# Kernel tuning notes

Measured on AMD Instinct MI355X. Metric: run time of the kernel, lower is better.

The kernel has to match this reference:

```python
import jax, jax.numpy as jnp
import numpy as np

D_MODEL = 256
D_IN = (D_MODEL + 1) ** 2  # 66049


def setup_inputs() -> dict:
    key = jax.random.key(0)
    k1, k2, k3, k4 = jax.random.split(key, 4)
    X = jax.random.normal(k1, (16, 256, 256), dtype=jnp.float32)
    X_aux = jax.random.normal(k2, (16, 256, 256), dtype=jnp.float32)
    # nn.Linear params: weight [out, in], bias [out]
    W = jax.random.normal(k3, (D_MODEL, D_IN), dtype=jnp.float32) / np.sqrt(D_IN)
    b = jax.random.normal(k4, (D_MODEL,), dtype=jnp.float32) * 0.01
    return {"X": X, "X_aux": X_aux, "W": W, "b": b}


def reference(X, X_aux, W, b):
    bsz, t, d = X.shape
    ones = jnp.ones((bsz, t, 1), dtype=X.dtype)
    Xa = jnp.concatenate([ones, X], axis=2)        # [b, t, d+1]
    Xb = jnp.concatenate([ones, X_aux], axis=2)    # [b, t, d+1]
    # outer product per (b, t): [b, t, d+1, d+1]
    tf = jnp.einsum("bti,btj->btij", Xa, Xb)
    tf = tf.reshape(bsz, t, -1)                    # [b, t, (d+1)^2]
    out = jnp.einsum("btk,ok->bto", tf, W) + b     # [b, t, d_model]
    return out
```

## Files before the change

### kernel.cpp

```cpp
#include <hip/hip_runtime.h>
#include <hip/hip_bf16.h>


#define DI 66049

typedef __attribute__((ext_vector_type(8))) short bf16x8;
typedef __attribute__((ext_vector_type(4))) float f32x4;

__device__ __forceinline__ unsigned short f2b(float f) {
  union { __hip_bfloat16 h; unsigned short u; } cv;
  cv.h = __float2bfloat16(f);
  return cv.u;
}

__device__ __forceinline__ bf16x8 pack8(f32x4 lo, f32x4 hi) {
  bf16x8 r;
  r[0] = (short)f2b(lo[0]); r[1] = (short)f2b(lo[1]);
  r[2] = (short)f2b(lo[2]); r[3] = (short)f2b(lo[3]);
  r[4] = (short)f2b(hi[0]); r[5] = (short)f2b(hi[1]);
  r[6] = (short)f2b(hi[2]); r[7] = (short)f2b(hi[3]);
  return r;
}

__device__ __forceinline__ void gload16(const void* g, void* l) {
  __builtin_amdgcn_global_load_lds(
      (const __attribute__((address_space(1))) unsigned int*)g,
      (__attribute__((address_space(3))) unsigned int*)l, 16, 0, 0);
}

__global__ void prep_w(const float* __restrict__ W, unsigned short* __restrict__ Bp) {
  const int c = blockIdx.x;
  const int o = (blockIdx.y << 2) + (threadIdx.x >> 6);
  const int j = (threadIdx.x & 63) << 2;
  const float* wrow = W + (size_t)o * DI;
  float v0, v1, v2, v3;
  if (c < 256) {
    const int bse = (c + 1) * 257 + 1 + j;
    v0 = wrow[bse]; v1 = wrow[bse + 1]; v2 = wrow[bse + 2]; v3 = wrow[bse + 3];
  } else if (c == 256) {
    const int bse = 1 + j;
    v0 = wrow[bse]; v1 = wrow[bse + 1]; v2 = wrow[bse + 2]; v3 = wrow[bse + 3];
  } else {
    v0 = wrow[(j + 1) * 257]; v1 = wrow[(j + 2) * 257];
    v2 = wrow[(j + 3) * 257]; v3 = wrow[(j + 4) * 257];
  }
  unsigned short* dst = Bp + (((size_t)c << 8) + o) * 256 + j;
  const unsigned int lo = (unsigned int)f2b(v0) | ((unsigned int)f2b(v1) << 16);
  const unsigned int hi = (unsigned int)f2b(v2) | ((unsigned int)f2b(v3) << 16);
  *(uint2*)dst = make_uint2(lo, hi);
}

__global__ void prep_xt(const float* __restrict__ X, float* __restrict__ Xt) {
  __shared__ float t[32][33];
  const int tx = threadIdx.x, ty = threadIdx.y;
  const int bt0 = blockIdx.x << 5, c0 = blockIdx.y << 5;
#pragma unroll
  for (int k = 0; k < 4; ++k) {
    const int row = (ty << 2) + k;
    t[row][tx] = X[(size_t)(bt0 + row) * 256 + c0 + tx];
  }
  __syncthreads();
#pragma unroll
  for (int k = 0; k < 4; ++k) {
    const int row = (ty << 2) + k;
    Xt[(size_t)(c0 + row) * 4096 + bt0 + tx] = t[tx][row];
  }
}

#define PACK_AS(SRC)                                                           \
  {                                                                            \
    const int _row = tid >> 2, _q = tid & 3;                                   \
    const float* _rp = (SRC) + (size_t)(bt0 + _row) * 256 + (_q << 6);         \
    const int _sx = _row & 15;                                                 \
    _Pragma("unroll") for (int _w = 0; _w < 8; ++_w) {                         \
      f32x4 _lo = *(const f32x4*)(_rp + (_w << 3));                            \
      f32x4 _hi = *(const f32x4*)(_rp + (_w << 3) + 4);                        \
      const int _slot = (_q << 3) + _w;                                        \
      *(bf16x8*)(&As[_row * 256 + ((_slot ^ _sx) << 3)]) = pack8(_lo, _hi);    \
    }                                                                          \
  }

#define LOAD_AFC()                                                             \
  {                                                                            \
    _Pragma("unroll") for (int _k4 = 0; _k4 < 2; ++_k4) {                      \
      _Pragma("unroll") for (int _rg = 0; _rg < 4; ++_rg) {                    \
        const int _ra = wr + (_rg << 4) + l15;                                 \
        const int _sx = _ra & 15;                                              \
        const int _sb = _k4 << 3;                                              \
        afc[_k4][_rg][0] =                                                     \
            *(const bf16x8*)(&As[_ra * 256 + (((_sb + lg) ^ _sx) << 3)]);      \
        afc[_k4][_rg][1] =                                                     \
            *(const bf16x8*)(&As[_ra * 256 + (((_sb + 4 + lg) ^ _sx) << 3)]);  \
      }                                                                        \
    }                                                                          \
  }

#define STAGE(C, JB, BUF)                                                      \
  {                                                                            \
    const unsigned _cb = ((unsigned)(C) << 16) + (unsigned)(JB);               \
    _Pragma("unroll") for (int _e = 0; _e < 4; ++_e) {                         \
      gload16(Bp + _cb + stg_off[_e],                                          \
              &Bs[BUF][(size_t)(((_e << 9) | tid)) << 3]);                     \
    }                                                                          \
  }

#define NEXT_CJ(K4, CN, JBN)                                                   \
  int _nk = (ci << 2) + (K4) + 1;                                              \
  if (_nk > nkmax) _nk = nkmax;                                                \
  const int _nci = _nk >> 2;                                                   \
  const int CN = is7 ? (_nci < 32 ? 225 + _nci : 257) : c0 + _nci;             \
  const int JBN = (_nk & 3) << 6;

#define KT(K4, CUR, A0X, A1X)                                                  \
  {                                                                            \
    NEXT_CJ(K4, _cn, _jbn);                                                    \
    STAGE(_cn, _jbn, (CUR) ^ 1);                                               \
    bf16x8 bf0[4], bf1[4];                                                     \
    _Pragma("unroll") for (int fn = 0; fn < 4; ++fn) {                         \
      const int _rb = (wn << 6) + (fn << 4) + l15;                             \
      const int _rx = _rb & 7;                                                 \
      bf0[fn] = *(const bf16x8*)(&Bs[CUR][_rb * 64 + ((lg ^ _rx) << 3)]);      \
      bf1[fn] = *(const bf16x8*)(&Bs[CUR][_rb * 64 + (((4 + lg) ^ _rx) << 3)]);\
    }                                                                          \
    _Pragma("unroll") for (int rg = 0; rg < 4; ++rg) {                         \
      bf16x8 _a0 = (A0X);                                                      \
      bf16x8 _a1 = (A1X);                                                      \
      _Pragma("unroll") for (int fn = 0; fn < 4; ++fn) {                       \
        t[rg][fn] = __builtin_amdgcn_mfma_f32_16x16x32_bf16(_a0, bf0[fn],      \
                                                            t[rg][fn], 0, 0, 0); \
        t[rg][fn] = __builtin_amdgcn_mfma_f32_16x16x32_bf16(_a1, bf1[fn],      \
                                                            t[rg][fn], 0, 0, 0); \
      }                                                                        \
    }                                                                          \
    __syncthreads();                                                           \
  }

#define ALDS(K4, HALF)                                                         \
  (*(const bf16x8*)(&As[(wr + (rg << 4) + l15) * 256 +                         \
                        (((((K4) << 3) + (HALF)*4 + lg) ^                      \
                          ((wr + (rg << 4) + l15) & 15))                       \
                         << 3)]))

__global__ __launch_bounds__(512, 1) void gemm_r8(
    const float* __restrict__ X, const float* __restrict__ Xb,
    const float* __restrict__ Xt, const unsigned short* __restrict__ Bp,
    float* __restrict__ P) {
  __shared__ __align__(16) unsigned short As[128 * 256];
  __shared__ __align__(16) unsigned short Bs[2][256 * 64];

  const int tid = threadIdx.x;
  const int rid = blockIdx.x;
  const int slice = rid & 7;
  const int bx = rid >> 3;
  const int bt0 = bx << 7;
  const bool is7 = (slice == 7);
  const int c0 = is7 ? 225 : slice * 32 + (slice ? 1 : 0);
  const int nCh = (slice == 0 || is7) ? 33 : 32;
  const int nkmax = (nCh << 2) - 1;

  const int wid = tid >> 6, lane = tid & 63;
  const int wm = wid >> 2, wn = wid & 3;
  const int wr = wm << 6;
  const int l15 = lane & 15, lg = lane >> 4;

  unsigned stg_off[4];
#pragma unroll
  for (int e = 0; e < 4; ++e) {
    const int row = (e << 6) | (tid >> 3);
    const int sl = (tid & 7) ^ (row & 7);
    stg_off[e] = (unsigned)(row * 256 + (sl << 3));
  }

  PACK_AS(Xb);
  STAGE(c0, 0, 0);
  __syncthreads();

  bf16x8 afc[2][4][2];
  LOAD_AFC();

  f32x4 acc[4][4] = {};

  for (int ci = 0; ci < nCh; ++ci) {
    const int c = is7 ? (ci < 32 ? 225 + ci : 257) : c0 + ci;

    f32x4 t[4][4] = {};
    KT(0, 0, afc[0][rg][0], afc[0][rg][1]);
    KT(1, 1, afc[1][rg][0], afc[1][rg][1]);
    KT(2, 0, ALDS(2, 0), ALDS(2, 1));
    KT(3, 1, ALDS(3, 0), ALDS(3, 1));

    f32x4 s4[4];
    if (c < 256) {
      const float* sp = Xt + (size_t)c * 4096 + bt0 + wr + (lg << 2);
#pragma unroll
      for (int rg = 0; rg < 4; ++rg) s4[rg] = *(const f32x4*)(sp + (rg << 4));
    } else {
#pragma unroll
      for (int rg = 0; rg < 4; ++rg) s4[rg] = (f32x4){1.f, 1.f, 1.f, 1.f};
    }
#pragma unroll
    for (int rg = 0; rg < 4; ++rg)
#pragma unroll
      for (int fn = 0; fn < 4; ++fn) acc[rg][fn] += s4[rg] * t[rg][fn];

    if (is7 && ci == 31) {
      __syncthreads();
      PACK_AS(X);
      __syncthreads();
      LOAD_AFC();
    }
  }

  float* pp = P + ((size_t)slice << 20);
#pragma unroll
  for (int rg = 0; rg < 4; ++rg) {
    const int row = bt0 + wr + (rg << 4) + (lg << 2);
#pragma unroll
    for (int fn = 0; fn < 4; ++fn) {
      const int col = (wn << 6) + (fn << 4) + l15;
#pragma unroll
      for (int e = 0; e < 4; ++e)
        pp[(size_t)(row + e) * 256 + col] = acc[rg][fn][e];
    }
  }
}

__global__ void reduce_k(const float* __restrict__ P, const float* __restrict__ W,
                         const float* __restrict__ b, float* __restrict__ out,
                         int nsl) {
  const int idx = blockIdx.x * 256 + threadIdx.x;
  const int o = idx & 255;
  float v = b[o] + W[(size_t)o * DI];
  for (int s = 0; s < nsl; ++s) v += P[idx + (size_t)s * 1048576];
  out[idx] = v;
}

__global__ void init_k(const float* __restrict__ W, const float* __restrict__ b,
                       float* __restrict__ out) {
  const int idx = blockIdx.x * 256 + threadIdx.x;
  const int o = idx & 255;
  out[idx] = b[o] + W[(size_t)o * DI];
}

__global__ __launch_bounds__(256, 4) void gemm_fb(
    const float* __restrict__ X, const float* __restrict__ Xa,
    const float* __restrict__ W, float* __restrict__ Out) {
  __shared__ __align__(16) unsigned short Asf[128 * 64];
  __shared__ __align__(16) unsigned short Bsf[128 * 64];
  const int tid = threadIdx.x;
  const int bx = blockIdx.x, by = blockIdx.y, bz = blockIdx.z;
  const int S = gridDim.z;
  const int bt0 = bx << 7, o0 = by << 7;
  const int q = 258 / S, r = 258 % S;
  const int c0 = bz * q + (bz < r ? bz : r);
  const int ccnt = q + (bz < r ? 1 : 0);
  const int nK = ccnt << 2;
  const int wid = tid >> 6, lane = tid & 63;
  const int wr = (wid >> 1) << 6, wc = (wid & 1) << 6;
  const int ar = tid >> 1;
  const int ah = (tid & 1) << 5;
  const float* xrow = X + (size_t)(bt0 + ar) * 256;
  const float* varow = Xa + (size_t)(bt0 + ar) * 256;
  f32x4 acc[4][4] = {};
  for (int kt = 0; kt < nK; ++kt) {
    const int c = c0 + (kt >> 2);
    const int j0 = (kt & 3) << 6;
    __syncthreads();
    {
      const float* vs = (c == 257) ? xrow : varow;
      float s = 1.0f;
      if (c < 256) s = xrow[c];
      const f32x4* vp = (const f32x4*)(vs + j0 + ah);
      f32x4 v[8];
#pragma unroll
      for (int qq = 0; qq < 8; ++qq) v[qq] = vp[qq];
      unsigned short* aw = Asf + ar * 64;
      const int sl0 = ah >> 3, sx = ar & 7;
#pragma unroll
      for (int w = 0; w < 4; ++w) {
        bf16x8 pk;
#pragma unroll
        for (int e = 0; e < 8; ++e)
          pk[e] = (short)f2b(s * v[w * 2 + (e >> 2)][e & 3]);
        *(bf16x8*)(aw + (((sl0 + w) ^ sx) << 3)) = pk;
      }
    }
    {
      const int orow = tid >> 1;
      const int jh = (tid & 1) << 5;
      const float* wrow = W + (size_t)(o0 + orow) * DI;
      float tmp[32];
      if (c < 256) {
        const int bse = (c + 1) * 257 + 1 + j0 + jh;
#pragma unroll
        for (int i = 0; i < 32; ++i) tmp[i] = wrow[bse + i];
      } else if (c == 256) {
        const int bse = 1 + j0 + jh;
#pragma unroll
        for (int i = 0; i < 32; ++i) tmp[i] = wrow[bse + i];
      } else {
#pragma unroll
        for (int i = 0; i < 32; ++i) tmp[i] = wrow[(j0 + jh + i + 1) * 257];
      }
      unsigned short* bw = Bsf + orow * 64;
      const int sl0 = jh >> 3, sx = orow & 7;
#pragma unroll
      for (int w = 0; w < 4; ++w) {
        bf16x8 pk;
#pragma unroll
        for (int e = 0; e < 8; ++e) pk[e] = (short)f2b(tmp[w * 8 + e]);
        *(bf16x8*)(bw + (((sl0 + w) ^ sx) << 3)) = pk;
      }
    }
    __syncthreads();
#pragma unroll
    for (int kk = 0; kk < 2; ++kk) {
      const int kslot = (kk << 2) + (lane >> 4);
      bf16x8 af[4], bfr2[4];
#pragma unroll
      for (int fm = 0; fm < 4; ++fm) {
        const int row = wr + (fm << 4) + (lane & 15);
        af[fm] = *(const bf16x8*)(Asf + row * 64 + ((kslot ^ (row & 7)) << 3));
      }
#pragma unroll
      for (int fn = 0; fn < 4; ++fn) {
        const int row = wc + (fn << 4) + (lane & 15);
        bfr2[fn] = *(const bf16x8*)(Bsf + row * 64 + ((kslot ^ (row & 7)) << 3));
      }
#pragma unroll
      for (int fm = 0; fm < 4; ++fm)
#pragma unroll
        for (int fn = 0; fn < 4; ++fn)
          acc[fm][fn] = __builtin_amdgcn_mfma_f32_16x16x32_bf16(
              af[fm], bfr2[fn], acc[fm][fn], 0, 0, 0);
    }
  }
  const int r0 = (lane >> 4) << 2;
  const int cl = lane & 15;
#pragma unroll
  for (int fm = 0; fm < 4; ++fm) {
    const int row = bt0 + wr + (fm << 4) + r0;
#pragma unroll
    for (int fn = 0; fn < 4; ++fn) {
      const int col = o0 + wc + (fn << 4) + cl;
#pragma unroll
      for (int rr = 0; rr < 4; ++rr)
        atomicAdd(Out + (size_t)(row + rr) * 256 + col, acc[fm][fn][rr]);
    }
  }
}

extern "C" void kernel_launch(void* const* d_in, const int* in_sizes, int n_in,
                              void* d_out, int out_size, void* d_ws, size_t ws_size,
                              hipStream_t stream) {
  const float* X  = (const float*)d_in[0];
  const float* Xa = (const float*)d_in[1];
  const float* W  = (const float*)d_in[2];
  const float* b  = (const float*)d_in[3];
  float* out = (float*)d_out;

  const size_t WBF_SZ = (size_t)258 * 256 * 256 * 2;
  const size_t XT_SZ  = (size_t)256 * 4096 * 4;
  const size_t PART1  = (size_t)4096 * 256 * 4;

  if (ws_size >= WBF_SZ + XT_SZ + 8 * PART1) {
    unsigned short* Bp = (unsigned short*)d_ws;
    float* Xt = (float*)((char*)d_ws + WBF_SZ);
    float* P  = (float*)((char*)d_ws + WBF_SZ + XT_SZ);
    prep_w<<<dim3(258, 64), 256, 0, stream>>>(W, Bp);
    prep_xt<<<dim3(128, 8), dim3(32, 8), 0, stream>>>(X, Xt);
    gemm_r8<<<dim3(256), 512, 0, stream>>>(X, Xa, Xt, Bp, P);
    reduce_k<<<4096, 256, 0, stream>>>(P, W, b, out, 8);
  } else {
    init_k<<<4096, 256, 0, stream>>>(W, b, out);
    gemm_fb<<<dim3(32, 2, 4), 256, 0, stream>>>(X, Xa, W, out);
  }
}
```

Measured before the change: 199.9 us.

## Restructure GEMM k-step sync with partial vmcnt waits, setprio, and LDS-cached scales

Each k-step now waits only until the previous tile's global-to-LDS loads have landed (s_waitcnt vmcnt(4)) and uses raw s_barrier calls, instead of a full __syncthreads after the MFMAs, so the next tile's prefetch can stay in flight. A fragments are reloaded from LDS every k-step rather than kept in registers, which frees VGPRs. The MFMA block is wrapped in s_setprio to favour matrix issue. The per-chunk Xt scale vectors are preloaded into a new LDS array once at kernel start, removing global loads from the inner loop at the cost of extra LDS traffic and about 17KB more shared memory.

```diff
diff --git a/kernel.cpp b/kernel.cpp
--- a/kernel.cpp
+++ b/kernel.cpp
@@ -80,21 +80,6 @@
     }                                                                          \
   }
 
-#define LOAD_AFC()                                                             \
-  {                                                                            \
-    _Pragma("unroll") for (int _k4 = 0; _k4 < 2; ++_k4) {                      \
-      _Pragma("unroll") for (int _rg = 0; _rg < 4; ++_rg) {                    \
-        const int _ra = wr + (_rg << 4) + l15;                                 \
-        const int _sx = _ra & 15;                                              \
-        const int _sb = _k4 << 3;                                              \
-        afc[_k4][_rg][0] =                                                     \
-            *(const bf16x8*)(&As[_ra * 256 + (((_sb + lg) ^ _sx) << 3)]);      \
-        afc[_k4][_rg][1] =                                                     \
-            *(const bf16x8*)(&As[_ra * 256 + (((_sb + 4 + lg) ^ _sx) << 3)]);  \
-      }                                                                        \
-    }                                                                          \
-  }
-
 #define STAGE(C, JB, BUF)                                                      \
   {                                                                            \
     const unsigned _cb = ((unsigned)(C) << 16) + (unsigned)(JB);               \
@@ -111,10 +96,12 @@
   const int CN = is7 ? (_nci < 32 ? 225 + _nci : 257) : c0 + _nci;             \
   const int JBN = (_nk & 3) << 6;
 
-#define KT(K4, CUR, A0X, A1X)                                                  \
+#define KT(K4, CUR, EXTRA)                                                     \
   {                                                                            \
     NEXT_CJ(K4, _cn, _jbn);                                                    \
     STAGE(_cn, _jbn, (CUR) ^ 1);                                               \
+    asm volatile("s_waitcnt vmcnt(4)" ::: "memory");                           \
+    __builtin_amdgcn_s_barrier();                                              \
     bf16x8 bf0[4], bf1[4];                                                     \
     _Pragma("unroll") for (int fn = 0; fn < 4; ++fn) {                         \
       const int _rb = (wn << 6) + (fn << 4) + l15;                             \
@@ -122,31 +109,35 @@
       bf0[fn] = *(const bf16x8*)(&Bs[CUR][_rb * 64 + ((lg ^ _rx) << 3)]);      \
       bf1[fn] = *(const bf16x8*)(&Bs[CUR][_rb * 64 + (((4 + lg) ^ _rx) << 3)]);\
     }                                                                          \
+    bf16x8 _aA[4], _aB[4];                                                     \
     _Pragma("unroll") for (int rg = 0; rg < 4; ++rg) {                         \
-      bf16x8 _a0 = (A0X);                                                      \
-      bf16x8 _a1 = (A1X);                                                      \
+      const int _ra = wr + (rg << 4) + l15;                                    \
+      const int _sx = _ra & 15;                                                \
+      _aA[rg] = *(const bf16x8*)(&As[_ra * 256 +                               \
+                                     (((((K4) << 3) + lg) ^ _sx) << 3)]);      \
+      _aB[rg] = *(const bf16x8*)(&As[_ra * 256 +                               \
+                                     (((((K4) << 3) + 4 + lg) ^ _sx) << 3)]);  \
+    }                                                                          \
+    EXTRA;                                                                     \
+    __builtin_amdgcn_s_setprio(1);                                             \
+    _Pragma("unroll") for (int rg = 0; rg < 4; ++rg)                           \
       _Pragma("unroll") for (int fn = 0; fn < 4; ++fn) {                       \
-        t[rg][fn] = __builtin_amdgcn_mfma_f32_16x16x32_bf16(_a0, bf0[fn],      \
-                                                            t[rg][fn], 0, 0, 0); \
-        t[rg][fn] = __builtin_amdgcn_mfma_f32_16x16x32_bf16(_a1, bf1[fn],      \
-                                                            t[rg][fn], 0, 0, 0); \
+        t[rg][fn] = __builtin_amdgcn_mfma_f32_16x16x32_bf16(                   \
+            _aA[rg], bf0[fn], t[rg][fn], 0, 0, 0);                             \
+        t[rg][fn] = __builtin_amdgcn_mfma_f32_16x16x32_bf16(                   \
+            _aB[rg], bf1[fn], t[rg][fn], 0, 0, 0);                             \
       }                                                                        \
-    }                                                                          \
-    __syncthreads();                                                           \
-  }
-
-#define ALDS(K4, HALF)                                                         \
-  (*(const bf16x8*)(&As[(wr + (rg << 4) + l15) * 256 +                         \
-                        (((((K4) << 3) + (HALF)*4 + lg) ^                      \
-                          ((wr + (rg << 4) + l15) & 15))                       \
-                         << 3)]))
-
-__global__ __launch_bounds__(512, 1) void gemm_r8(
+    __builtin_amdgcn_s_setprio(0);                                             \
+    __builtin_amdgcn_s_barrier();                                              \
+  }
+
+__global__ __launch_bounds__(512, 1) void gemm_r9(
     const float* __restrict__ X, const float* __restrict__ Xb,
     const float* __restrict__ Xt, const unsigned short* __restrict__ Bp,
     float* __restrict__ P) {
   __shared__ __align__(16) unsigned short As[128 * 256];
   __shared__ __align__(16) unsigned short Bs[2][256 * 64];
+  __shared__ __align__(16) float Ss[33 * 128];
 
   const int tid = threadIdx.x;
   const int rid = blockIdx.x;
@@ -172,32 +163,26 @@
   }
 
   PACK_AS(Xb);
+  for (int i = tid; i < (nCh << 7); i += 512) {
+    const int ci = i >> 7, r = i & 127;
+    const int c = is7 ? (ci < 32 ? 225 + ci : 257) : c0 + ci;
+    Ss[i] = (c < 256) ? Xt[(size_t)c * 4096 + bt0 + r] : 1.0f;
+  }
   STAGE(c0, 0, 0);
   __syncthreads();
 
-  bf16x8 afc[2][4][2];
-  LOAD_AFC();
-
   f32x4 acc[4][4] = {};
 
   for (int ci = 0; ci < nCh; ++ci) {
-    const int c = is7 ? (ci < 32 ? 225 + ci : 257) : c0 + ci;
-
     f32x4 t[4][4] = {};
-    KT(0, 0, afc[0][rg][0], afc[0][rg][1]);
-    KT(1, 1, afc[1][rg][0], afc[1][rg][1]);
-    KT(2, 0, ALDS(2, 0), ALDS(2, 1));
-    KT(3, 1, ALDS(3, 0), ALDS(3, 1));
-
     f32x4 s4[4];
-    if (c < 256) {
-      const float* sp = Xt + (size_t)c * 4096 + bt0 + wr + (lg << 2);
-#pragma unroll
-      for (int rg = 0; rg < 4; ++rg) s4[rg] = *(const f32x4*)(sp + (rg << 4));
-    } else {
-#pragma unroll
-      for (int rg = 0; rg < 4; ++rg) s4[rg] = (f32x4){1.f, 1.f, 1.f, 1.f};
-    }
+    KT(0, 0, {});
+    KT(1, 1, {});
+    KT(2, 0, {});
+    KT(3, 1, {
+      _Pragma("unroll") for (int rg = 0; rg < 4; ++rg)
+          s4[rg] = *(const f32x4*)(&Ss[(ci << 7) + wr + (rg << 4) + (lg << 2)]);
+    });
 #pragma unroll
     for (int rg = 0; rg < 4; ++rg)
 #pragma unroll
@@ -207,7 +192,6 @@
       __syncthreads();
       PACK_AS(X);
       __syncthreads();
-      LOAD_AFC();
     }
   }
 
@@ -369,7 +353,7 @@
     float* P  = (float*)((char*)d_ws + WBF_SZ + XT_SZ);
     prep_w<<<dim3(258, 64), 256, 0, stream>>>(W, Bp);
     prep_xt<<<dim3(128, 8), dim3(32, 8), 0, stream>>>(X, Xt);
-    gemm_r8<<<dim3(256), 512, 0, stream>>>(X, Xa, Xt, Bp, P);
+    gemm_r9<<<dim3(256), 512, 0, stream>>>(X, Xa, Xt, Bp, P);
     reduce_k<<<4096, 256, 0, stream>>>(P, W, b, out, 8);
   } else {
     init_k<<<4096, 256, 0, stream>>>(W, b, out);
```

Result: faster. 183.8 us (-8.1%).
